# Performance work log

Hardware: AMD Instinct MI355X
Metric: run time of the kernel (lower is better)

The kernel has to match this reference:

```python
import jax, jax.numpy as jnp
import numpy as np

NUM_EXPERTS = 8
TOP_K = 2
B, S, H, I = 4, 2048, 2048, 1408
INIT = 0.02


def setup_inputs() -> dict:
    key = jax.random.key(0)
    ks = jax.random.split(key, 6)
    return {
        "selected_experts": jax.random.randint(ks[0], (B, S, TOP_K), 0, NUM_EXPERTS, dtype=jnp.int32),
        "hidden_states": jax.random.normal(ks[1], (B, S, H), dtype=jnp.float32),
        "routing_weights": jax.random.uniform(ks[2], (B, S, TOP_K), dtype=jnp.float32),
        "gate_w": jax.random.normal(ks[3], (NUM_EXPERTS, H, I), dtype=jnp.float32) * INIT,
        "up_w": jax.random.normal(ks[4], (NUM_EXPERTS, H, I), dtype=jnp.float32) * INIT,
        "down_w": jax.random.normal(ks[5], (NUM_EXPERTS, I, H), dtype=jnp.float32) * INIT,
        "batch_size": B,
        "sequence_length": S,
        "hidden_dim": H,
    }


def reference(selected_experts, hidden_states, routing_weights, gate_w, up_w, down_w,
              batch_size, sequence_length, hidden_dim):
    # Naive MoE: every expert's SwiGLU MLP runs on every token, then the
    # output is scaled by sum((selected_experts == e) * routing_weights, -1).
    num_experts = gate_w.shape[0]
    final = jnp.zeros_like(hidden_states)
    for e in range(num_experts):  # fixed small expert count, structurally a loop in the original
        g = jnp.einsum("bsh,hi->bsi", hidden_states, gate_w[e])
        u = jnp.einsum("bsh,hi->bsi", hidden_states, up_w[e])
        out = jnp.einsum("bsi,ih->bsh", jax.nn.silu(g) * u, down_w[e])
        w = jnp.sum(jnp.where(selected_experts == e, routing_weights, 0.0), axis=-1)  # [B,S]
        final = final + w[:, :, None] * out
    return final
```

## Files before the change

### kernel.cpp

```cpp
#include <hip/hip_runtime.h>
#include <stdint.h>

#define TT 8192
#define HH 2048
#define II 1408
#define NE 8
#define NROWS (TT*2)
#define BM 128
#define BK 64
#define BN 128
#define MAX_SLOTS 144
#define NKT_GU (HH/BK)
#define NKT_DN (II/BK)
#define NYT_GU (II/BN)
#define NYT_DN (HH/BN)
#define SLOTS_PER_XCD (MAX_SLOTS/8)

typedef unsigned short u16;
typedef __attribute__((ext_vector_type(8))) __bf16 bhalf8;
typedef __attribute__((ext_vector_type(4))) float f32x4;
typedef __attribute__((ext_vector_type(4))) float float4v;
typedef __attribute__((ext_vector_type(4))) int int4v;

__device__ __forceinline__ u16 f2bf(float f) {
  union { float f; unsigned u; } v; v.f = f;
  return (u16)((v.u + 0x7FFFu + ((v.u >> 16) & 1u)) >> 16);
}

__device__ __forceinline__ void gld16(const void* g, void* l) {
  __builtin_amdgcn_global_load_lds(
      (const __attribute__((address_space(1))) unsigned int*)g,
      (__attribute__((address_space(3))) unsigned int*)l, 16, 0, 0);
}

__global__ __launch_bounds__(256) void k_cvt_hs(const float* __restrict__ in,
                                                u16* __restrict__ out) {
  size_t i = ((size_t)blockIdx.x * 256 + threadIdx.x) * 8;
  float4v a = *(const float4v*)(in + i);
  float4v b = *(const float4v*)(in + i + 4);
  u16 o[8];
  o[0] = f2bf(a.x); o[1] = f2bf(a.y); o[2] = f2bf(a.z); o[3] = f2bf(a.w);
  o[4] = f2bf(b.x); o[5] = f2bf(b.y); o[6] = f2bf(b.z); o[7] = f2bf(b.w);
  *(int4v*)(out + i) = *(const int4v*)o;
}

__global__ __launch_bounds__(256) void k_tconv(const float* __restrict__ in,
                                               u16* __restrict__ out,
                                               int R, int C) {
  __shared__ float t[64][65];
  int e = blockIdx.z;
  int r0 = blockIdx.y * 64, c0 = blockIdx.x * 64;
  const float* ip = in + (size_t)e * R * C;
  u16* op = out + (size_t)e * R * C;
  int tid = threadIdx.x;
  int rr = tid >> 4, c4 = (tid & 15) * 4;
#pragma unroll
  for (int j = 0; j < 4; ++j) {
    float4v v = *(const float4v*)&ip[(size_t)(r0 + rr + 16 * j) * C + c0 + c4];
    t[rr + 16 * j][c4 + 0] = v.x;
    t[rr + 16 * j][c4 + 1] = v.y;
    t[rr + 16 * j][c4 + 2] = v.z;
    t[rr + 16 * j][c4 + 3] = v.w;
  }
  __syncthreads();
  int cc = tid >> 2, rb = (tid & 3) * 16;
  u16 buf[16];
#pragma unroll
  for (int i = 0; i < 16; ++i) buf[i] = f2bf(t[rb + i][cc]);
  u16* p = op + (size_t)(c0 + cc) * R + r0 + rb;
  *(int4v*)p = *(const int4v*)&buf[0];
  *(int4v*)(p + 8) = *(const int4v*)&buf[8];
}

__global__ __launch_bounds__(256) void k_route(const int* __restrict__ sel,
                                               const float* __restrict__ rw,
                                               int* __restrict__ token_idx,
                                               float* __restrict__ wrow,
                                               int* __restrict__ s_e,
                                               int* __restrict__ s_rs,
                                               int* __restrict__ s_rows) {
  __shared__ int cnt[NE], offs[NE + 1], cursor[NE];
  int tid = threadIdx.x;
  if (tid < NE) cnt[tid] = 0;
  __syncthreads();
  for (int i = tid; i < NROWS; i += 256) atomicAdd(&cnt[sel[i]], 1);
  __syncthreads();
  if (tid == 0) {
    int o = 0;
    for (int e = 0; e < NE; ++e) { offs[e] = o; o += cnt[e]; }
    offs[NE] = o;
    int ns = 0;
    for (int e = 0; e < NE; ++e) {
      for (int t = 0; t < cnt[e]; t += BM) {
        s_e[ns] = e;
        s_rs[ns] = offs[e] + t;
        s_rows[ns] = (cnt[e] - t < BM) ? (cnt[e] - t) : BM;
        ns++;
      }
    }
    for (; ns < MAX_SLOTS; ++ns) s_rows[ns] = 0;
  }
  __syncthreads();
  if (tid < NE) cursor[tid] = offs[tid];
  __syncthreads();
  for (int i = tid; i < NROWS; i += 256) {
    int e = sel[i];
    int r = atomicAdd(&cursor[e], 1);
    token_idx[r] = i >> 1;
    wrow[r] = rw[i];
  }
}

__global__ __launch_bounds__(256, 2) void k_gu(const u16* __restrict__ hsb,
                                               const u16* __restrict__ gwt,
                                               const u16* __restrict__ uwt,
                                               const int* __restrict__ token_idx,
                                               const float* __restrict__ wrow,
                                               const int* __restrict__ s_e,
                                               const int* __restrict__ s_rs,
                                               const int* __restrict__ s_rows,
                                               u16* __restrict__ act) {
  int f = blockIdx.x;
  int xcd = f & 7;
  int pos = f >> 3;
  int slot = xcd * SLOTS_PER_XCD + pos / NYT_GU;
  int ytile = pos % NYT_GU;
  int nrows = s_rows[slot];
  if (nrows == 0) return;
  int e = s_e[slot];
  int row0 = s_rs[slot];
  int i0 = ytile * BN;

  __shared__ alignas(16) u16 As[BM][BK];
  __shared__ alignas(16) u16 Bg[BN][BK];
  __shared__ alignas(16) u16 Bu[BN][BK];

  int tid = threadIdx.x;
  int lane = tid & 63;
  int wid = tid >> 6;
  int l8 = lane >> 3;
  int c8 = lane & 7;
  int cs = c8 ^ l8;

  const u16* agp[4];
#pragma unroll
  for (int j = 0; j < 4; ++j) {
    int gr = row0 + wid * 32 + j * 8 + l8;
    if (gr > NROWS - 1) gr = NROWS - 1;
    int tok = token_idx[gr];
    agp[j] = hsb + (size_t)tok * HH + cs * 8;
  }
  const u16* ggp[4]; const u16* ugp[4];
#pragma unroll
  for (int j = 0; j < 4; ++j) {
    size_t off = ((size_t)e * II + i0 + wid * 32 + j * 8 + l8) * HH + cs * 8;
    ggp[j] = gwt + off;
    ugp[j] = uwt + off;
  }

  int wm = wid >> 1, wn = wid & 1;
  int l15 = lane & 15, l16 = lane >> 4;

  f32x4 accg[4][4], accu[4][4];
#pragma unroll
  for (int a = 0; a < 4; ++a)
#pragma unroll
    for (int b = 0; b < 4; ++b) { accg[a][b] = (f32x4)0.0f; accu[a][b] = (f32x4)0.0f; }

  for (int kt = 0; kt < NKT_GU; ++kt) {
    int k0 = kt * BK;
#pragma unroll
    for (int j = 0; j < 4; ++j) {
      gld16(agp[j] + k0, &As[wid * 32 + j * 8][0]);
      gld16(ggp[j] + k0, &Bg[wid * 32 + j * 8][0]);
      gld16(ugp[j] + k0, &Bu[wid * 32 + j * 8][0]);
    }
    __syncthreads();
#pragma unroll
    for (int ks = 0; ks < 2; ++ks) {
      bhalf8 af[4], bgf[4], buf_[4];
#pragma unroll
      for (int mf = 0; mf < 4; ++mf) {
        int row = wm * 64 + mf * 16 + l15;
        int c = (ks * 4 + l16) ^ (row & 7);
        af[mf] = *(const bhalf8*)&As[row][c * 8];
      }
#pragma unroll
      for (int nf = 0; nf < 4; ++nf) {
        int row = wn * 64 + nf * 16 + l15;
        int c = (ks * 4 + l16) ^ (row & 7);
        bgf[nf] = *(const bhalf8*)&Bg[row][c * 8];
        buf_[nf] = *(const bhalf8*)&Bu[row][c * 8];
      }
      __builtin_amdgcn_s_setprio(1);
#pragma unroll
      for (int mf = 0; mf < 4; ++mf)
#pragma unroll
        for (int nf = 0; nf < 4; ++nf) {
          accg[mf][nf] = __builtin_amdgcn_mfma_f32_16x16x32_bf16(af[mf], bgf[nf], accg[mf][nf], 0, 0, 0);
          accu[mf][nf] = __builtin_amdgcn_mfma_f32_16x16x32_bf16(af[mf], buf_[nf], accu[mf][nf], 0, 0, 0);
        }
      __builtin_amdgcn_s_setprio(0);
    }
    __syncthreads();
  }

#pragma unroll
  for (int mf = 0; mf < 4; ++mf) {
#pragma unroll
    for (int j = 0; j < 4; ++j) {
      int lm = wm * 64 + mf * 16 + l16 * 4 + j;
      if (lm < nrows) {
        int gr = row0 + lm;
        float w = wrow[gr];
        size_t base = (size_t)gr * II + i0 + wn * 64 + l15;
#pragma unroll
        for (int nf = 0; nf < 4; ++nf) {
          float g = accg[mf][nf][j];
          float u = accu[mf][nf][j];
          float s = g / (1.0f + __expf(-g));
          act[base + nf * 16] = f2bf(s * u * w);
        }
      }
    }
  }
}

__global__ __launch_bounds__(256, 3) void k_down(const u16* __restrict__ act,
                                                 const u16* __restrict__ dwt,
                                                 const int* __restrict__ token_idx,
                                                 const int* __restrict__ s_e,
                                                 const int* __restrict__ s_rs,
                                                 const int* __restrict__ s_rows,
                                                 float* __restrict__ out) {
  int f = blockIdx.x;
  int xcd = f & 7;
  int pos = f >> 3;
  int slot = xcd * SLOTS_PER_XCD + pos / NYT_DN;
  int ytile = pos % NYT_DN;
  int nrows = s_rows[slot];
  if (nrows == 0) return;
  int e = s_e[slot];
  int row0 = s_rs[slot];
  int h0 = ytile * BN;

  __shared__ alignas(16) u16 As[BM][BK];
  __shared__ alignas(16) u16 Bs[BN][BK];

  int tid = threadIdx.x;
  int lane = tid & 63;
  int wid = tid >> 6;
  int l8 = lane >> 3;
  int c8 = lane & 7;
  int cs = c8 ^ l8;

  const u16* agp[4];
#pragma unroll
  for (int j = 0; j < 4; ++j) {
    int gr = row0 + wid * 32 + j * 8 + l8;
    if (gr > NROWS - 1) gr = NROWS - 1;
    agp[j] = act + (size_t)gr * II + cs * 8;
  }
  const u16* bgp[4];
#pragma unroll
  for (int j = 0; j < 4; ++j)
    bgp[j] = dwt + ((size_t)e * HH + h0 + wid * 32 + j * 8 + l8) * II + cs * 8;

  int wm = wid >> 1, wn = wid & 1;
  int l15 = lane & 15, l16 = lane >> 4;

  f32x4 acc[4][4];
#pragma unroll
  for (int a = 0; a < 4; ++a)
#pragma unroll
    for (int b = 0; b < 4; ++b) acc[a][b] = (f32x4)0.0f;

  for (int kt = 0; kt < NKT_DN; ++kt) {
    int k0 = kt * BK;
#pragma unroll
    for (int j = 0; j < 4; ++j) {
      gld16(agp[j] + k0, &As[wid * 32 + j * 8][0]);
      gld16(bgp[j] + k0, &Bs[wid * 32 + j * 8][0]);
    }
    __syncthreads();
#pragma unroll
    for (int ks = 0; ks < 2; ++ks) {
      bhalf8 af[4], bf[4];
#pragma unroll
      for (int mf = 0; mf < 4; ++mf) {
        int row = wm * 64 + mf * 16 + l15;
        int c = (ks * 4 + l16) ^ (row & 7);
        af[mf] = *(const bhalf8*)&As[row][c * 8];
      }
#pragma unroll
      for (int nf = 0; nf < 4; ++nf) {
        int row = wn * 64 + nf * 16 + l15;
        int c = (ks * 4 + l16) ^ (row & 7);
        bf[nf] = *(const bhalf8*)&Bs[row][c * 8];
      }
      __builtin_amdgcn_s_setprio(1);
#pragma unroll
      for (int mf = 0; mf < 4; ++mf)
#pragma unroll
        for (int nf = 0; nf < 4; ++nf)
          acc[mf][nf] = __builtin_amdgcn_mfma_f32_16x16x32_bf16(af[mf], bf[nf], acc[mf][nf], 0, 0, 0);
      __builtin_amdgcn_s_setprio(0);
    }
    __syncthreads();
  }

#pragma unroll
  for (int mf = 0; mf < 4; ++mf) {
#pragma unroll
    for (int j = 0; j < 4; ++j) {
      int lm = wm * 64 + mf * 16 + l16 * 4 + j;
      if (lm < nrows) {
        int tok = token_idx[row0 + lm];
        size_t base = (size_t)tok * HH + h0 + wn * 64 + l15;
#pragma unroll
        for (int nf = 0; nf < 4; ++nf)
          atomicAdd(&out[base + nf * 16], acc[mf][nf][j]);
      }
    }
  }
}

extern "C" void kernel_launch(void* const* d_in, const int* in_sizes, int n_in,
                              void* d_out, int out_size, void* d_ws, size_t ws_size,
                              hipStream_t stream) {
  const int* sel = (const int*)d_in[0];
  const float* hs = (const float*)d_in[1];
  const float* rw = (const float*)d_in[2];
  const float* gw = (const float*)d_in[3];
  const float* uw = (const float*)d_in[4];
  const float* dw = (const float*)d_in[5];
  float* out = (float*)d_out;

  char* ws = (char*)d_ws;
  size_t o = 0;
  u16* hsb = (u16*)(ws + o); o += (size_t)TT * HH * 2;
  u16* gwt = (u16*)(ws + o); o += (size_t)NE * HH * II * 2;
  u16* uwt = (u16*)(ws + o); o += (size_t)NE * HH * II * 2;
  u16* dwt = (u16*)(ws + o); o += (size_t)NE * HH * II * 2;
  u16* act = (u16*)(ws + o); o += (size_t)NROWS * II * 2;
  int* token_idx = (int*)(ws + o); o += (size_t)NROWS * 4;
  float* wrow = (float*)(ws + o); o += (size_t)NROWS * 4;
  int* s_e = (int*)(ws + o); o += MAX_SLOTS * 4;
  int* s_rs = (int*)(ws + o); o += MAX_SLOTS * 4;
  int* s_rows = (int*)(ws + o); o += MAX_SLOTS * 4;
  (void)ws_size; (void)in_sizes; (void)n_in; (void)out_size;

  k_cvt_hs<<<(TT * HH) / 2048, 256, 0, stream>>>(hs, hsb);
  dim3 g1(II / 64, HH / 64, NE);
  k_tconv<<<g1, 256, 0, stream>>>(gw, gwt, HH, II);
  k_tconv<<<g1, 256, 0, stream>>>(uw, uwt, HH, II);
  dim3 g2(HH / 64, II / 64, NE);
  k_tconv<<<g2, 256, 0, stream>>>(dw, dwt, II, HH);

  k_route<<<1, 256, 0, stream>>>(sel, rw, token_idx, wrow, s_e, s_rs, s_rows);
  hipMemsetAsync(d_out, 0, (size_t)TT * HH * 4, stream);

  k_gu<<<MAX_SLOTS * NYT_GU, 256, 0, stream>>>(hsb, gwt, uwt, token_idx, wrow,
                                               s_e, s_rs, s_rows, act);

  k_down<<<MAX_SLOTS * NYT_DN, 256, 0, stream>>>(act, dwt, token_idx,
                                                 s_e, s_rs, s_rows, out);
}
```

Baseline: 598.5 us.

## Interleave gate/up weights and add triple-buffered 512-thread GEMM pipeline

Gate and up weights are transposed into a single interleaved buffer, in 16-column groups, so one 256-wide B tile covers both projections and each block runs a single accumulator set. Both grouped GEMM kernels move to 512 threads in 8 waves with a 128x256 tile. The K loop now uses three LDS stages, prefetching two tiles ahead and issuing the global-to-LDS loads in small slices between MFMA groups, with explicit vmcnt waits and raw barriers. The goal is to hide global load latency and cut synchronisation stalls. In exchange it uses more LDS per block and many more barriers per K step, and it depends on the vmcnt counts being exactly right.

```diff
diff --git a/kernel.cpp b/kernel.cpp
--- a/kernel.cpp
+++ b/kernel.cpp
@@ -4,17 +4,18 @@
 #define TT 8192
 #define HH 2048
 #define II 1408
+#define IIC (II*2)
 #define NE 8
 #define NROWS (TT*2)
 #define BM 128
 #define BK 64
-#define BN 128
+#define BNC 256
 #define MAX_SLOTS 144
 #define NKT_GU (HH/BK)
 #define NKT_DN (II/BK)
-#define NYT_GU (II/BN)
-#define NYT_DN (HH/BN)
-#define SLOTS_PER_XCD (MAX_SLOTS/8)
+#define NYT_GU (IIC/BNC)
+#define NYT_DN (HH/BNC)
+#define SPX (MAX_SLOTS/8)
 
 typedef unsigned short u16;
 typedef __attribute__((ext_vector_type(8))) __bf16 bhalf8;
@@ -31,6 +32,12 @@
   __builtin_amdgcn_global_load_lds(
       (const __attribute__((address_space(1))) unsigned int*)g,
       (__attribute__((address_space(3))) unsigned int*)l, 16, 0, 0);
+}
+
+__device__ __forceinline__ void barrier_raw() {
+  asm volatile("" ::: "memory");
+  __builtin_amdgcn_s_barrier();
+  asm volatile("" ::: "memory");
 }
 
 __global__ __launch_bounds__(256) void k_cvt_hs(const float* __restrict__ in,
@@ -68,6 +75,37 @@
 #pragma unroll
   for (int i = 0; i < 16; ++i) buf[i] = f2bf(t[rb + i][cc]);
   u16* p = op + (size_t)(c0 + cc) * R + r0 + rb;
+  *(int4v*)p = *(const int4v*)&buf[0];
+  *(int4v*)(p + 8) = *(const int4v*)&buf[8];
+}
+
+__global__ __launch_bounds__(256) void k_tconv_gu(const float* __restrict__ in,
+                                                  u16* __restrict__ out,
+                                                  int is_up) {
+  __shared__ float t[64][65];
+  const int R = HH, C = II;
+  int e = blockIdx.z;
+  int r0 = blockIdx.y * 64, c0 = blockIdx.x * 64;
+  const float* ip = in + (size_t)e * R * C;
+  u16* op = out + (size_t)e * IIC * R;
+  int tid = threadIdx.x;
+  int rr = tid >> 4, c4 = (tid & 15) * 4;
+#pragma unroll
+  for (int j = 0; j < 4; ++j) {
+    float4v v = *(const float4v*)&ip[(size_t)(r0 + rr + 16 * j) * C + c0 + c4];
+    t[rr + 16 * j][c4 + 0] = v.x;
+    t[rr + 16 * j][c4 + 1] = v.y;
+    t[rr + 16 * j][c4 + 2] = v.z;
+    t[rr + 16 * j][c4 + 3] = v.w;
+  }
+  __syncthreads();
+  int cc = tid >> 2, rb = (tid & 3) * 16;
+  u16 buf[16];
+#pragma unroll
+  for (int i = 0; i < 16; ++i) buf[i] = f2bf(t[rb + i][cc]);
+  int c = c0 + cc;
+  int crow = ((c >> 4) << 5) + (is_up << 4) + (c & 15);
+  u16* p = op + (size_t)crow * R + r0 + rb;
   *(int4v*)p = *(const int4v*)&buf[0];
   *(int4v*)(p + 8) = *(const int4v*)&buf[8];
 }
@@ -111,98 +149,129 @@
   }
 }
 
-__global__ __launch_bounds__(256, 2) void k_gu(const u16* __restrict__ hsb,
-                                               const u16* __restrict__ gwt,
-                                               const u16* __restrict__ uwt,
-                                               const int* __restrict__ token_idx,
-                                               const float* __restrict__ wrow,
-                                               const int* __restrict__ s_e,
-                                               const int* __restrict__ s_rs,
-                                               const int* __restrict__ s_rows,
-                                               u16* __restrict__ act) {
+__global__ __launch_bounds__(512) void k_gu(const u16* __restrict__ hsb,
+                                            const u16* __restrict__ guw,
+                                            const int* __restrict__ token_idx,
+                                            const float* __restrict__ wrow,
+                                            const int* __restrict__ s_e,
+                                            const int* __restrict__ s_rs,
+                                            const int* __restrict__ s_rows,
+                                            u16* __restrict__ act) {
   int f = blockIdx.x;
-  int xcd = f & 7;
-  int pos = f >> 3;
-  int slot = xcd * SLOTS_PER_XCD + pos / NYT_GU;
+  int xcd = f & 7, pos = f >> 3;
+  int slot = xcd * SPX + pos / NYT_GU;
   int ytile = pos % NYT_GU;
   int nrows = s_rows[slot];
   if (nrows == 0) return;
-  int e = s_e[slot];
-  int row0 = s_rs[slot];
-  int i0 = ytile * BN;
-
-  __shared__ alignas(16) u16 As[BM][BK];
-  __shared__ alignas(16) u16 Bg[BN][BK];
-  __shared__ alignas(16) u16 Bu[BN][BK];
-
-  int tid = threadIdx.x;
-  int lane = tid & 63;
-  int wid = tid >> 6;
-  int l8 = lane >> 3;
-  int c8 = lane & 7;
-  int cs = c8 ^ l8;
-
-  const u16* agp[4];
+  int e = s_e[slot], row0 = s_rs[slot];
+  int i0c = ytile * BNC;
+  int i0r = ytile * 128;
+
+  __shared__ alignas(16) u16 As[3][BM][BK];
+  __shared__ alignas(16) u16 Bs[3][BNC][BK];
+
+  int tid = threadIdx.x, lane = tid & 63, wid = tid >> 6;
+  int l8 = lane >> 3, c8 = lane & 7, cs = c8 ^ l8;
+  int wm = wid >> 2, wn = wid & 3;
+  int l15 = lane & 15, l16 = lane >> 4;
+  int cswz = l16 ^ (l15 & 7);
+
+  const u16* agp[2];
+#pragma unroll
+  for (int j = 0; j < 2; ++j) {
+    int gr = row0 + wid * 16 + j * 8 + l8;
+    if (gr > NROWS - 1) gr = NROWS - 1;
+    agp[j] = hsb + (size_t)token_idx[gr] * HH + cs * 8;
+  }
+  const u16* bgp[4];
 #pragma unroll
   for (int j = 0; j < 4; ++j) {
-    int gr = row0 + wid * 32 + j * 8 + l8;
-    if (gr > NROWS - 1) gr = NROWS - 1;
-    int tok = token_idx[gr];
-    agp[j] = hsb + (size_t)tok * HH + cs * 8;
-  }
-  const u16* ggp[4]; const u16* ugp[4];
-#pragma unroll
-  for (int j = 0; j < 4; ++j) {
-    size_t off = ((size_t)e * II + i0 + wid * 32 + j * 8 + l8) * HH + cs * 8;
-    ggp[j] = gwt + off;
-    ugp[j] = uwt + off;
-  }
-
-  int wm = wid >> 1, wn = wid & 1;
-  int l15 = lane & 15, l16 = lane >> 4;
-
-  f32x4 accg[4][4], accu[4][4];
+    int brow = i0c + wid * 32 + j * 8 + l8;
+    bgp[j] = guw + ((size_t)e * IIC + brow) * HH + cs * 8;
+  }
+
+  f32x4 acc[4][4];
 #pragma unroll
   for (int a = 0; a < 4; ++a)
 #pragma unroll
-    for (int b = 0; b < 4; ++b) { accg[a][b] = (f32x4)0.0f; accu[a][b] = (f32x4)0.0f; }
-
-  for (int kt = 0; kt < NKT_GU; ++kt) {
-    int k0 = kt * BK;
-#pragma unroll
-    for (int j = 0; j < 4; ++j) {
-      gld16(agp[j] + k0, &As[wid * 32 + j * 8][0]);
-      gld16(ggp[j] + k0, &Bg[wid * 32 + j * 8][0]);
-      gld16(ugp[j] + k0, &Bu[wid * 32 + j * 8][0]);
-    }
-    __syncthreads();
-#pragma unroll
-    for (int ks = 0; ks < 2; ++ks) {
-      bhalf8 af[4], bgf[4], buf_[4];
-#pragma unroll
-      for (int mf = 0; mf < 4; ++mf) {
-        int row = wm * 64 + mf * 16 + l15;
-        int c = (ks * 4 + l16) ^ (row & 7);
-        af[mf] = *(const bhalf8*)&As[row][c * 8];
-      }
-#pragma unroll
-      for (int nf = 0; nf < 4; ++nf) {
-        int row = wn * 64 + nf * 16 + l15;
-        int c = (ks * 4 + l16) ^ (row & 7);
-        bgf[nf] = *(const bhalf8*)&Bg[row][c * 8];
-        buf_[nf] = *(const bhalf8*)&Bu[row][c * 8];
-      }
-      __builtin_amdgcn_s_setprio(1);
-#pragma unroll
-      for (int mf = 0; mf < 4; ++mf)
-#pragma unroll
-        for (int nf = 0; nf < 4; ++nf) {
-          accg[mf][nf] = __builtin_amdgcn_mfma_f32_16x16x32_bf16(af[mf], bgf[nf], accg[mf][nf], 0, 0, 0);
-          accu[mf][nf] = __builtin_amdgcn_mfma_f32_16x16x32_bf16(af[mf], buf_[nf], accu[mf][nf], 0, 0, 0);
-        }
-      __builtin_amdgcn_s_setprio(0);
-    }
-    __syncthreads();
+    for (int b = 0; b < 4; ++b) acc[a][b] = (f32x4)0.0f;
+
+#pragma unroll
+  for (int j = 0; j < 2; ++j) gld16(agp[j], &As[0][wid * 16 + j * 8][0]);
+#pragma unroll
+  for (int j = 0; j < 4; ++j) gld16(bgp[j], &Bs[0][wid * 32 + j * 8][0]);
+#pragma unroll
+  for (int j = 0; j < 2; ++j) gld16(agp[j] + BK, &As[1][wid * 16 + j * 8][0]);
+#pragma unroll
+  for (int j = 0; j < 4; ++j) gld16(bgp[j] + BK, &Bs[1][wid * 32 + j * 8][0]);
+
+  for (int t = 0; t < NKT_GU; ++t) {
+    int cb = t % 3;
+    int sb = cb + 2; if (sb >= 3) sb -= 3;
+    int kn = (t + 2) * BK;
+    bool dost = (t + 2 < NKT_GU);
+    if (t == NKT_GU - 1) asm volatile("s_waitcnt vmcnt(0)" ::: "memory");
+    else                 asm volatile("s_waitcnt vmcnt(6)" ::: "memory");
+    barrier_raw();
+
+    bhalf8 af[4], bf[4];
+#pragma unroll
+    for (int mf = 0; mf < 4; ++mf)
+      af[mf] = *(const bhalf8*)&As[cb][wm * 64 + mf * 16 + l15][cswz * 8];
+    bf[0] = *(const bhalf8*)&Bs[cb][wn * 64 + 0 + l15][cswz * 8];
+    bf[1] = *(const bhalf8*)&Bs[cb][wn * 64 + 16 + l15][cswz * 8];
+    if (dost) { gld16(agp[0] + kn, &As[sb][wid * 16 + 0][0]);
+                gld16(bgp[0] + kn, &Bs[sb][wid * 32 + 0][0]); }
+    barrier_raw();
+    __builtin_amdgcn_s_setprio(1);
+#pragma unroll
+    for (int mf = 0; mf < 4; ++mf) {
+      acc[mf][0] = __builtin_amdgcn_mfma_f32_16x16x32_bf16(af[mf], bf[0], acc[mf][0], 0, 0, 0);
+      acc[mf][1] = __builtin_amdgcn_mfma_f32_16x16x32_bf16(af[mf], bf[1], acc[mf][1], 0, 0, 0);
+    }
+    __builtin_amdgcn_s_setprio(0);
+    barrier_raw();
+    bf[2] = *(const bhalf8*)&Bs[cb][wn * 64 + 32 + l15][cswz * 8];
+    bf[3] = *(const bhalf8*)&Bs[cb][wn * 64 + 48 + l15][cswz * 8];
+    if (dost) { gld16(agp[1] + kn, &As[sb][wid * 16 + 8][0]);
+                gld16(bgp[1] + kn, &Bs[sb][wid * 32 + 8][0]); }
+    barrier_raw();
+    __builtin_amdgcn_s_setprio(1);
+#pragma unroll
+    for (int mf = 0; mf < 4; ++mf) {
+      acc[mf][2] = __builtin_amdgcn_mfma_f32_16x16x32_bf16(af[mf], bf[2], acc[mf][2], 0, 0, 0);
+      acc[mf][3] = __builtin_amdgcn_mfma_f32_16x16x32_bf16(af[mf], bf[3], acc[mf][3], 0, 0, 0);
+    }
+    __builtin_amdgcn_s_setprio(0);
+    barrier_raw();
+    int cz1 = cswz ^ 4;
+#pragma unroll
+    for (int mf = 0; mf < 4; ++mf)
+      af[mf] = *(const bhalf8*)&As[cb][wm * 64 + mf * 16 + l15][cz1 * 8];
+    bf[0] = *(const bhalf8*)&Bs[cb][wn * 64 + 0 + l15][cz1 * 8];
+    bf[1] = *(const bhalf8*)&Bs[cb][wn * 64 + 16 + l15][cz1 * 8];
+    if (dost) gld16(bgp[2] + kn, &Bs[sb][wid * 32 + 16][0]);
+    barrier_raw();
+    __builtin_amdgcn_s_setprio(1);
+#pragma unroll
+    for (int mf = 0; mf < 4; ++mf) {
+      acc[mf][0] = __builtin_amdgcn_mfma_f32_16x16x32_bf16(af[mf], bf[0], acc[mf][0], 0, 0, 0);
+      acc[mf][1] = __builtin_amdgcn_mfma_f32_16x16x32_bf16(af[mf], bf[1], acc[mf][1], 0, 0, 0);
+    }
+    __builtin_amdgcn_s_setprio(0);
+    barrier_raw();
+    bf[2] = *(const bhalf8*)&Bs[cb][wn * 64 + 32 + l15][cz1 * 8];
+    bf[3] = *(const bhalf8*)&Bs[cb][wn * 64 + 48 + l15][cz1 * 8];
+    if (dost) gld16(bgp[3] + kn, &Bs[sb][wid * 32 + 24][0]);
+    barrier_raw();
+    __builtin_amdgcn_s_setprio(1);
+#pragma unroll
+    for (int mf = 0; mf < 4; ++mf) {
+      acc[mf][2] = __builtin_amdgcn_mfma_f32_16x16x32_bf16(af[mf], bf[2], acc[mf][2], 0, 0, 0);
+      acc[mf][3] = __builtin_amdgcn_mfma_f32_16x16x32_bf16(af[mf], bf[3], acc[mf][3], 0, 0, 0);
+    }
+    __builtin_amdgcn_s_setprio(0);
+    barrier_raw();
   }
 
 #pragma unroll
@@ -213,61 +282,57 @@
       if (lm < nrows) {
         int gr = row0 + lm;
         float w = wrow[gr];
-        size_t base = (size_t)gr * II + i0 + wn * 64 + l15;
-#pragma unroll
-        for (int nf = 0; nf < 4; ++nf) {
-          float g = accg[mf][nf][j];
-          float u = accu[mf][nf][j];
+        size_t base = (size_t)gr * II + i0r + wn * 32 + l15;
+#pragma unroll
+        for (int t2 = 0; t2 < 2; ++t2) {
+          float g = acc[mf][2 * t2][j];
+          float u = acc[mf][2 * t2 + 1][j];
           float s = g / (1.0f + __expf(-g));
-          act[base + nf * 16] = f2bf(s * u * w);
+          act[base + t2 * 16] = f2bf(s * u * w);
         }
       }
     }
   }
 }
 
-__global__ __launch_bounds__(256, 3) void k_down(const u16* __restrict__ act,
-                                                 const u16* __restrict__ dwt,
-                                                 const int* __restrict__ token_idx,
-                                                 const int* __restrict__ s_e,
-                                                 const int* __restrict__ s_rs,
-                                                 const int* __restrict__ s_rows,
-                                                 float* __restrict__ out) {
+__global__ __launch_bounds__(512) void k_down(const u16* __restrict__ act,
+                                              const u16* __restrict__ dwt,
+                                              const int* __restrict__ token_idx,
+                                              const int* __restrict__ s_e,
+                                              const int* __restrict__ s_rs,
+                                              const int* __restrict__ s_rows,
+                                              float* __restrict__ out) {
   int f = blockIdx.x;
-  int xcd = f & 7;
-  int pos = f >> 3;
-  int slot = xcd * SLOTS_PER_XCD + pos / NYT_DN;
+  int xcd = f & 7, pos = f >> 3;
+  int slot = xcd * SPX + pos / NYT_DN;
   int ytile = pos % NYT_DN;
   int nrows = s_rows[slot];
   if (nrows == 0) return;
-  int e = s_e[slot];
-  int row0 = s_rs[slot];
-  int h0 = ytile * BN;
-
-  __shared__ alignas(16) u16 As[BM][BK];
-  __shared__ alignas(16) u16 Bs[BN][BK];
-
-  int tid = threadIdx.x;
-  int lane = tid & 63;
-  int wid = tid >> 6;
-  int l8 = lane >> 3;
-  int c8 = lane & 7;
-  int cs = c8 ^ l8;
-
-  const u16* agp[4];
-#pragma unroll
-  for (int j = 0; j < 4; ++j) {
-    int gr = row0 + wid * 32 + j * 8 + l8;
+  int e = s_e[slot], row0 = s_rs[slot];
+  int h0 = ytile * BNC;
+
+  __shared__ alignas(16) u16 As[3][BM][BK];
+  __shared__ alignas(16) u16 Bs[3][BNC][BK];
+
+  int tid = threadIdx.x, lane = tid & 63, wid = tid >> 6;
+  int l8 = lane >> 3, c8 = lane & 7, cs = c8 ^ l8;
+  int wm = wid >> 2, wn = wid & 3;
+  int l15 = lane & 15, l16 = lane >> 4;
+  int cswz = l16 ^ (l15 & 7);
+
+  const u16* agp[2];
+#pragma unroll
+  for (int j = 0; j < 2; ++j) {
+    int gr = row0 + wid * 16 + j * 8 + l8;
     if (gr > NROWS - 1) gr = NROWS - 1;
     agp[j] = act + (size_t)gr * II + cs * 8;
   }
   const u16* bgp[4];
 #pragma unroll
-  for (int j = 0; j < 4; ++j)
-    bgp[j] = dwt + ((size_t)e * HH + h0 + wid * 32 + j * 8 + l8) * II + cs * 8;
-
-  int wm = wid >> 1, wn = wid & 1;
-  int l15 = lane & 15, l16 = lane >> 4;
+  for (int j = 0; j < 4; ++j) {
+    int brow = h0 + wid * 32 + j * 8 + l8;
+    bgp[j] = dwt + ((size_t)e * HH + brow) * II + cs * 8;
+  }
 
   f32x4 acc[4][4];
 #pragma unroll
@@ -275,38 +340,82 @@
 #pragma unroll
     for (int b = 0; b < 4; ++b) acc[a][b] = (f32x4)0.0f;
 
-  for (int kt = 0; kt < NKT_DN; ++kt) {
-    int k0 = kt * BK;
-#pragma unroll
-    for (int j = 0; j < 4; ++j) {
-      gld16(agp[j] + k0, &As[wid * 32 + j * 8][0]);
-      gld16(bgp[j] + k0, &Bs[wid * 32 + j * 8][0]);
-    }
-    __syncthreads();
-#pragma unroll
-    for (int ks = 0; ks < 2; ++ks) {
-      bhalf8 af[4], bf[4];
-#pragma unroll
-      for (int mf = 0; mf < 4; ++mf) {
-        int row = wm * 64 + mf * 16 + l15;
-        int c = (ks * 4 + l16) ^ (row & 7);
-        af[mf] = *(const bhalf8*)&As[row][c * 8];
-      }
-#pragma unroll
-      for (int nf = 0; nf < 4; ++nf) {
-        int row = wn * 64 + nf * 16 + l15;
-        int c = (ks * 4 + l16) ^ (row & 7);
-        bf[nf] = *(const bhalf8*)&Bs[row][c * 8];
-      }
-      __builtin_amdgcn_s_setprio(1);
-#pragma unroll
-      for (int mf = 0; mf < 4; ++mf)
-#pragma unroll
-        for (int nf = 0; nf < 4; ++nf)
-          acc[mf][nf] = __builtin_amdgcn_mfma_f32_16x16x32_bf16(af[mf], bf[nf], acc[mf][nf], 0, 0, 0);
-      __builtin_amdgcn_s_setprio(0);
-    }
-    __syncthreads();
+#pragma unroll
+  for (int j = 0; j < 2; ++j) gld16(agp[j], &As[0][wid * 16 + j * 8][0]);
+#pragma unroll
+  for (int j = 0; j < 4; ++j) gld16(bgp[j], &Bs[0][wid * 32 + j * 8][0]);
+#pragma unroll
+  for (int j = 0; j < 2; ++j) gld16(agp[j] + BK, &As[1][wid * 16 + j * 8][0]);
+#pragma unroll
+  for (int j = 0; j < 4; ++j) gld16(bgp[j] + BK, &Bs[1][wid * 32 + j * 8][0]);
+
+  for (int t = 0; t < NKT_DN; ++t) {
+    int cb = t % 3;
+    int sb = cb + 2; if (sb >= 3) sb -= 3;
+    int kn = (t + 2) * BK;
+    bool dost = (t + 2 < NKT_DN);
+    if (t == NKT_DN - 1) asm volatile("s_waitcnt vmcnt(0)" ::: "memory");
+    else                 asm volatile("s_waitcnt vmcnt(6)" ::: "memory");
+    barrier_raw();
+
+    bhalf8 af[4], bf[4];
+#pragma unroll
+    for (int mf = 0; mf < 4; ++mf)
+      af[mf] = *(const bhalf8*)&As[cb][wm * 64 + mf * 16 + l15][cswz * 8];
+    bf[0] = *(const bhalf8*)&Bs[cb][wn * 64 + 0 + l15][cswz * 8];
+    bf[1] = *(const bhalf8*)&Bs[cb][wn * 64 + 16 + l15][cswz * 8];
+    if (dost) { gld16(agp[0] + kn, &As[sb][wid * 16 + 0][0]);
+                gld16(bgp[0] + kn, &Bs[sb][wid * 32 + 0][0]); }
+    barrier_raw();
+    __builtin_amdgcn_s_setprio(1);
+#pragma unroll
+    for (int mf = 0; mf < 4; ++mf) {
+      acc[mf][0] = __builtin_amdgcn_mfma_f32_16x16x32_bf16(af[mf], bf[0], acc[mf][0], 0, 0, 0);
+      acc[mf][1] = __builtin_amdgcn_mfma_f32_16x16x32_bf16(af[mf], bf[1], acc[mf][1], 0, 0, 0);
+    }
+    __builtin_amdgcn_s_setprio(0);
+    barrier_raw();
+    bf[2] = *(const bhalf8*)&Bs[cb][wn * 64 + 32 + l15][cswz * 8];
+    bf[3] = *(const bhalf8*)&Bs[cb][wn * 64 + 48 + l15][cswz * 8];
+    if (dost) { gld16(agp[1] + kn, &As[sb][wid * 16 + 8][0]);
+                gld16(bgp[1] + kn, &Bs[sb][wid * 32 + 8][0]); }
+    barrier_raw();
+    __builtin_amdgcn_s_setprio(1);
+#pragma unroll
+    for (int mf = 0; mf < 4; ++mf) {
+      acc[mf][2] = __builtin_amdgcn_mfma_f32_16x16x32_bf16(af[mf], bf[2], acc[mf][2], 0, 0, 0);
+      acc[mf][3] = __builtin_amdgcn_mfma_f32_16x16x32_bf16(af[mf], bf[3], acc[mf][3], 0, 0, 0);
+    }
+    __builtin_amdgcn_s_setprio(0);
+    barrier_raw();
+    int cz1 = cswz ^ 4;
+#pragma unroll
+    for (int mf = 0; mf < 4; ++mf)
+      af[mf] = *(const bhalf8*)&As[cb][wm * 64 + mf * 16 + l15][cz1 * 8];
+    bf[0] = *(const bhalf8*)&Bs[cb][wn * 64 + 0 + l15][cz1 * 8];
+    bf[1] = *(const bhalf8*)&Bs[cb][wn * 64 + 16 + l15][cz1 * 8];
+    if (dost) gld16(bgp[2] + kn, &Bs[sb][wid * 32 + 16][0]);
+    barrier_raw();
+    __builtin_amdgcn_s_setprio(1);
+#pragma unroll
+    for (int mf = 0; mf < 4; ++mf) {
+      acc[mf][0] = __builtin_amdgcn_mfma_f32_16x16x32_bf16(af[mf], bf[0], acc[mf][0], 0, 0, 0);
+      acc[mf][1] = __builtin_amdgcn_mfma_f32_16x16x32_bf16(af[mf], bf[1], acc[mf][1], 0, 0, 0);
+    }
+    __builtin_amdgcn_s_setprio(0);
+    barrier_raw();
+    bf[2] = *(const bhalf8*)&Bs[cb][wn * 64 + 32 + l15][cz1 * 8];
+    bf[3] = *(const bhalf8*)&Bs[cb][wn * 64 + 48 + l15][cz1 * 8];
+    if (dost) gld16(bgp[3] + kn, &Bs[sb][wid * 32 + 24][0]);
+    barrier_raw();
+    __builtin_amdgcn_s_setprio(1);
+#pragma unroll
+    for (int mf = 0; mf < 4; ++mf) {
+      acc[mf][2] = __builtin_amdgcn_mfma_f32_16x16x32_bf16(af[mf], bf[2], acc[mf][2], 0, 0, 0);
+      acc[mf][3] = __builtin_amdgcn_mfma_f32_16x16x32_bf16(af[mf], bf[3], acc[mf][3], 0, 0, 0);
+    }
+    __builtin_amdgcn_s_setprio(0);
+    barrier_raw();
   }
 
 #pragma unroll
@@ -339,8 +448,7 @@
   char* ws = (char*)d_ws;
   size_t o = 0;
   u16* hsb = (u16*)(ws + o); o += (size_t)TT * HH * 2;
-  u16* gwt = (u16*)(ws + o); o += (size_t)NE * HH * II * 2;
-  u16* uwt = (u16*)(ws + o); o += (size_t)NE * HH * II * 2;
+  u16* guw = (u16*)(ws + o); o += (size_t)NE * IIC * HH * 2;
   u16* dwt = (u16*)(ws + o); o += (size_t)NE * HH * II * 2;
   u16* act = (u16*)(ws + o); o += (size_t)NROWS * II * 2;
   int* token_idx = (int*)(ws + o); o += (size_t)NROWS * 4;
@@ -352,17 +460,17 @@
 
   k_cvt_hs<<<(TT * HH) / 2048, 256, 0, stream>>>(hs, hsb);
   dim3 g1(II / 64, HH / 64, NE);
-  k_tconv<<<g1, 256, 0, stream>>>(gw, gwt, HH, II);
-  k_tconv<<<g1, 256, 0, stream>>>(uw, uwt, HH, II);
+  k_tconv_gu<<<g1, 256, 0, stream>>>(gw, guw, 0);
+  k_tconv_gu<<<g1, 256, 0, stream>>>(uw, guw, 1);
   dim3 g2(HH / 64, II / 64, NE);
   k_tconv<<<g2, 256, 0, stream>>>(dw, dwt, II, HH);
 
   k_route<<<1, 256, 0, stream>>>(sel, rw, token_idx, wrow, s_e, s_rs, s_rows);
   hipMemsetAsync(d_out, 0, (size_t)TT * HH * 4, stream);
 
-  k_gu<<<MAX_SLOTS * NYT_GU, 256, 0, stream>>>(hsb, gwt, uwt, token_idx, wrow,
+  k_gu<<<MAX_SLOTS * NYT_GU, 512, 0, stream>>>(hsb, guw, token_idx, wrow,
                                                s_e, s_rs, s_rows, act);
 
-  k_down<<<MAX_SLOTS * NYT_DN, 256, 0, stream>>>(act, dwt, token_idx,
+  k_down<<<MAX_SLOTS * NYT_DN, 512, 0, stream>>>(act, dwt, token_idx,
                                                  s_e, s_rs, s_rows, out);
 }
```

After: 806.2 us. 34.7% more time.
